# Performance work log

Measured on AMD Instinct MI355X. Metric: run time of the kernel, lower is better.

## Reference

```python
import math
import jax, jax.numpy as jnp
import numpy as np

B, T, M, D = 65536, 20, 4, 4   # batch, timesteps, regions, d_reg
L, H, FF = 3, 2, 16            # layers, heads, dim_feedforward
S = M + 1                      # seq_len with cls token
TAU = 10000.0


def setup_inputs() -> dict:
    key = jax.random.key(0)
    ks = jax.random.split(key, 8)

    def w(k, shape, std=0.1):
        return jax.random.normal(k, shape, dtype=jnp.float32) * std

    return {
        "regional_states": jax.random.normal(ks[0], (B, T, M, D), dtype=jnp.float32),
        "cls_token": w(ks[1], (1, 1, D), 0.02),
        # stacked per-layer params (layer axis first)
        "Wqkv": w(ks[2], (L, 3 * D, D)),   # nn.MultiheadAttention in_proj_weight
        "bqkv": jnp.zeros((L, 3 * D), jnp.float32),
        "Wo": w(ks[3], (L, D, D)),          # out_proj weight
        "bo": jnp.zeros((L, D), jnp.float32),
        "W1": w(ks[4], (L, FF, D)),         # linear1 weight (torch layout: out, in)
        "b1": jnp.zeros((L, FF), jnp.float32),
        "W2": w(ks[5], (L, D, FF)),         # linear2 weight
        "b2": jnp.zeros((L, D), jnp.float32),
    }


def _positional_encoding():
    # PE(pos,2i)=sin(pos/tau^(2i/D)), PE(pos,2i+1)=cos(...)
    pos = jnp.arange(S, dtype=jnp.float32)[:, None]            # (S,1)
    div = jnp.exp(jnp.arange(0, D, 2, dtype=jnp.float32) * (-math.log(TAU) / D))
    pe = jnp.zeros((S, D), jnp.float32)
    pe = pe.at[:, 0::2].set(jnp.sin(pos * div))
    pe = pe.at[:, 1::2].set(jnp.cos(pos * div))
    return pe  # (S, D)


def _layer(x, Wqkv, bqkv, Wo, bo, W1, b1, W2, b2):
    # x: (N, S, D). Dropout is identity (eval mode).
    N, Sq, Dm = x.shape
    hd = Dm // H
    qkv = x @ Wqkv.T + bqkv                     # (N, S, 3D)
    q, k, v = jnp.split(qkv, 3, axis=-1)

    def heads(t):
        return t.reshape(N, Sq, H, hd).transpose(0, 2, 1, 3)  # (N, H, S, hd)

    q, k, v = heads(q), heads(k), heads(v)
    scores = jnp.einsum("nhqd,nhkd->nhqk", q, k) / math.sqrt(hd)
    attn = jax.nn.softmax(scores, axis=-1)
    o = jnp.einsum("nhqk,nhkd->nhqd", attn, v)
    o = o.transpose(0, 2, 1, 3).reshape(N, Sq, Dm)
    attn_out = o @ Wo.T + bo
    x = x + attn_out                            # residual (no norm)
    ff = jax.nn.relu(x @ W1.T + b1) @ W2.T + b2
    return x + ff


def reference(regional_states, cls_token, Wqkv, bqkv, Wo, bo, W1, b1, W2, b2):
    Bq, Tq, Mq, Dq = regional_states.shape
    N = Bq * Tq
    x = regional_states.reshape(N, Mq, Dq)
    cls = jnp.broadcast_to(cls_token, (N, 1, Dq))
    x = jnp.concatenate([cls, x], axis=1)       # (N, S, D)
    x = x + _positional_encoding()[None, :, :]
    for i in range(L):
        x = _layer(x, Wqkv[i], bqkv[i], Wo[i], bo[i], W1[i], b1[i], W2[i], b2[i])
    F_g = x[:, 0, :].reshape(Bq, Tq, Dq)
    subregion_seq = x[:, 1:, :].reshape(Bq, Tq, Mq * Dq)
    return (F_g, subregion_seq)
```

## Files before the change

### kernel.cpp

```cpp
#include <hip/hip_runtime.h>


enum {
  OFF_CLS  = 0,
  OFF_WQKV = 4,
  OFF_BQKV = 148,
  OFF_WO   = 184,
  OFF_BO   = 232,
  OFF_W1   = 244,
  OFF_B1   = 436,
  OFF_W2   = 484,
  OFF_B2   = 676,
  WF_TOTAL = 688,
  FLAG_XF32 = 688
};

__device__ __forceinline__ float bf2f(unsigned short u) {
  unsigned int x = ((unsigned int)u) << 16;
  float f;
  __builtin_memcpy(&f, &x, 4);
  return f;
}

__device__ __forceinline__ bool is_bf16_packed(const unsigned int* w) {
  int pass = 0;
#pragma unroll
  for (int i = 0; i < 16; ++i) {
    unsigned int lo = w[i] & 0xFFFFu;
    unsigned int e = (lo >> 7) & 0xFFu;
    if (lo == 0u || (e >= 90u && e <= 140u)) ++pass;
  }
  return pass >= 15;
}

__global__ void mpt_prep(const void* __restrict__ cls,
                         const void* __restrict__ Wqkv,
                         const void* __restrict__ bqkv,
                         const void* __restrict__ Wo,
                         const void* __restrict__ bo,
                         const void* __restrict__ W1,
                         const void* __restrict__ b1,
                         const void* __restrict__ W2,
                         const void* __restrict__ b2,
                         const void* __restrict__ xin,
                         float* __restrict__ wf) {
  const bool wbf = is_bf16_packed((const unsigned int*)Wqkv);
  const bool xbf = is_bf16_packed((const unsigned int*)xin);
  if (threadIdx.x == 0) ((int*)wf)[FLAG_XF32] = xbf ? 0 : 1;
  for (int i = threadIdx.x; i < WF_TOTAL; i += 256) {
    const void* src;
    int k;
    if      (i < OFF_WQKV) { src = cls;  k = i - OFF_CLS;  }
    else if (i < OFF_BQKV) { src = Wqkv; k = i - OFF_WQKV; }
    else if (i < OFF_WO)   { src = bqkv; k = i - OFF_BQKV; }
    else if (i < OFF_BO)   { src = Wo;   k = i - OFF_WO;   }
    else if (i < OFF_W1)   { src = bo;   k = i - OFF_BO;   }
    else if (i < OFF_B1)   { src = W1;   k = i - OFF_W1;   }
    else if (i < OFF_W2)   { src = b1;   k = i - OFF_B1;   }
    else if (i < OFF_B2)   { src = W2;   k = i - OFF_W2;   }
    else                   { src = b2;   k = i - OFF_B2;   }
    wf[i] = wbf ? bf2f(((const unsigned short*)src)[k])
                : ((const float*)src)[k];
  }
}

__global__ __launch_bounds__(256) void mpt_main(
    const void* __restrict__ xin,
    const float* __restrict__ wf,
    float* __restrict__ out,
    int N) {
  const int n = blockIdx.x * 256 + threadIdx.x;
  if (n >= N) return;

  const int xf32 = ((const int*)wf)[FLAG_XF32];

  const float pe[5][4] = {
    { 0.0f,                1.0f,                0.0f,                1.0f               },
    { 0.8414709848078965f, 0.5403023058681398f, 0.0099998333341667f, 0.9999500004166653f },
    { 0.9092974268256817f,-0.4161468365471424f, 0.0199986666933331f, 0.9998000066665778f },
    { 0.1411200080598672f,-0.9899924966004454f, 0.0299955002024957f, 0.9995500337489875f },
    {-0.7568024953079283f,-0.6536436208636119f, 0.0399893341866342f, 0.9992001066609779f }
  };

  float raw[16];
  if (xf32) {
    const float4* pf = reinterpret_cast<const float4*>((const float*)xin + (size_t)n * 16);
#pragma unroll
    for (int r = 0; r < 4; ++r) {
      float4 t = pf[r];
      raw[r * 4 + 0] = t.x; raw[r * 4 + 1] = t.y;
      raw[r * 4 + 2] = t.z; raw[r * 4 + 3] = t.w;
    }
  } else {
    struct alignas(16) U8 { unsigned short v[8]; };
    const U8* p = reinterpret_cast<const U8*>((const unsigned short*)xin + (size_t)n * 16);
    U8 a0 = p[0], a1 = p[1];
#pragma unroll
    for (int j = 0; j < 8; ++j) {
      raw[j]     = bf2f(a0.v[j]);
      raw[8 + j] = bf2f(a1.v[j]);
    }
  }

  float x[5][4];
#pragma unroll
  for (int d = 0; d < 4; ++d) x[0][d] = wf[OFF_CLS + d] + pe[0][d];
#pragma unroll
  for (int r = 0; r < 4; ++r)
#pragma unroll
    for (int d = 0; d < 4; ++d) x[1 + r][d] = raw[r * 4 + d] + pe[1 + r][d];

  const float scale = 0.70710678118654752f;

#pragma unroll
  for (int l = 0; l < 3; ++l) {
    const float* Wqkv = wf + OFF_WQKV + l * 48;
    const float* bqkv = wf + OFF_BQKV + l * 12;
    const float* Wo   = wf + OFF_WO   + l * 16;
    const float* bo   = wf + OFF_BO   + l * 4;
    const float* W1   = wf + OFF_W1   + l * 64;
    const float* b1   = wf + OFF_B1   + l * 16;
    const float* W2   = wf + OFF_W2   + l * 64;
    const float* b2   = wf + OFF_B2   + l * 4;

    float q[5][4], k[5][4], v[5][4];
#pragma unroll
    for (int s = 0; s < 5; ++s) {
#pragma unroll
      for (int j = 0; j < 12; ++j) {
        float a = bqkv[j];
#pragma unroll
        for (int d = 0; d < 4; ++d) a = fmaf(x[s][d], Wqkv[j * 4 + d], a);
        if (j < 4)      q[s][j] = a;
        else if (j < 8) k[s][j - 4] = a;
        else            v[s][j - 8] = a;
      }
    }

    float o[5][4];
#pragma unroll
    for (int h = 0; h < 2; ++h) {
      const int d0 = 2 * h, d1 = 2 * h + 1;
#pragma unroll
      for (int si = 0; si < 5; ++si) {
        float sc[5];
        float mx = -3.0e38f;
#pragma unroll
        for (int sj = 0; sj < 5; ++sj) {
          float s0 = q[si][d0] * k[sj][d0] + q[si][d1] * k[sj][d1];
          sc[sj] = s0 * scale;
          mx = fmaxf(mx, sc[sj]);
        }
        float den = 0.f, o0 = 0.f, o1 = 0.f;
#pragma unroll
        for (int sj = 0; sj < 5; ++sj) {
          float e = __expf(sc[sj] - mx);
          den += e;
          o0 = fmaf(e, v[sj][d0], o0);
          o1 = fmaf(e, v[sj][d1], o1);
        }
        float inv = __builtin_amdgcn_rcpf(den);
        o[si][d0] = o0 * inv;
        o[si][d1] = o1 * inv;
      }
    }

#pragma unroll
    for (int s = 0; s < 5; ++s) {
      float nx[4];
#pragma unroll
      for (int i = 0; i < 4; ++i) {
        float a = bo[i];
#pragma unroll
        for (int j = 0; j < 4; ++j) a = fmaf(o[s][j], Wo[i * 4 + j], a);
        nx[i] = x[s][i] + a;
      }
#pragma unroll
      for (int i = 0; i < 4; ++i) x[s][i] = nx[i];

      float acc[4] = {b2[0], b2[1], b2[2], b2[3]};
#pragma unroll
      for (int f = 0; f < 16; ++f) {
        float hs = b1[f];
#pragma unroll
        for (int d = 0; d < 4; ++d) hs = fmaf(x[s][d], W1[f * 4 + d], hs);
        hs = fmaxf(hs, 0.f);
#pragma unroll
        for (int i = 0; i < 4; ++i) acc[i] = fmaf(hs, W2[i * 16 + f], acc[i]);
      }
#pragma unroll
      for (int i = 0; i < 4; ++i) x[s][i] += acc[i];
    }
  }

  float4 fg = make_float4(x[0][0], x[0][1], x[0][2], x[0][3]);
  *reinterpret_cast<float4*>(out + (size_t)n * 4) = fg;

  float* sub = out + (size_t)N * 4 + (size_t)n * 16;
#pragma unroll
  for (int r = 0; r < 4; ++r) {
    float4 t = make_float4(x[1 + r][0], x[1 + r][1], x[1 + r][2], x[1 + r][3]);
    *reinterpret_cast<float4*>(sub + r * 4) = t;
  }
}

extern "C" void kernel_launch(void* const* d_in, const int* in_sizes, int n_in,
                              void* d_out, int out_size, void* d_ws, size_t ws_size,
                              hipStream_t stream) {
  float* wf = (float*)d_ws;

  mpt_prep<<<1, 256, 0, stream>>>(
      d_in[1],
      d_in[2],
      d_in[3],
      d_in[4],
      d_in[5],
      d_in[6],
      d_in[7],
      d_in[8],
      d_in[9],
      d_in[0],
      wf);

  const int N = in_sizes[0] / 16;
  mpt_main<<<(N + 255) / 256, 256, 0, stream>>>(
      d_in[0], wf, (float*)d_out, N);
}
```

Measured before the change: 296.9 us.

## Process two sequences per thread with packed float2 math and prescaled keys

Each thread now handles two sequences packed into float2 vectors, so the compiler can emit packed FMA (v_pk_fma_f32) instructions. Weights are duplicated into float2 pairs in the workspace, and the key projection is prescaled by 1/sqrt(hd) in the prep kernel. The softmax max-subtraction is dropped, and Q/K/V projections are recomputed per head rather than stored. The aim is to halve VALU instruction count, at the cost of more registers per thread, half as many threads, and possible exp overflow without the max shift.

```diff
diff --git a/kernel.cpp b/kernel.cpp
--- a/kernel.cpp
+++ b/kernel.cpp
@@ -1,5 +1,7 @@
 #include <hip/hip_runtime.h>
 
+
+typedef float f2 __attribute__((ext_vector_type(2)));
 
 enum {
   OFF_CLS  = 0,
@@ -12,7 +14,7 @@
   OFF_W2   = 484,
   OFF_B2   = 676,
   WF_TOTAL = 688,
-  FLAG_XF32 = 688
+  FLAG_IDX = 2 * WF_TOTAL
 };
 
 __device__ __forceinline__ float bf2f(unsigned short u) {
@@ -46,7 +48,8 @@
                          float* __restrict__ wf) {
   const bool wbf = is_bf16_packed((const unsigned int*)Wqkv);
   const bool xbf = is_bf16_packed((const unsigned int*)xin);
-  if (threadIdx.x == 0) ((int*)wf)[FLAG_XF32] = xbf ? 0 : 1;
+  if (threadIdx.x == 0) ((int*)wf)[FLAG_IDX] = xbf ? 0 : 1;
+  const float scale = 0.70710678118654752f;
   for (int i = threadIdx.x; i < WF_TOTAL; i += 256) {
     const void* src;
     int k;
@@ -59,20 +62,59 @@
     else if (i < OFF_W2)   { src = b1;   k = i - OFF_B1;   }
     else if (i < OFF_B2)   { src = W2;   k = i - OFF_W2;   }
     else                   { src = b2;   k = i - OFF_B2;   }
-    wf[i] = wbf ? bf2f(((const unsigned short*)src)[k])
-                : ((const float*)src)[k];
-  }
+    float val = wbf ? bf2f(((const unsigned short*)src)[k])
+                    : ((const float*)src)[k];
+    if (i >= OFF_WQKV && i < OFF_BQKV) {
+      int kk = i - OFF_WQKV;
+      int row = (kk % 48) / 4;
+      if (row >= 4 && row < 8) val *= scale;
+    } else if (i >= OFF_BQKV && i < OFF_WO) {
+      int j = (i - OFF_BQKV) % 12;
+      if (j >= 4 && j < 8) val *= scale;
+    }
+    wf[2 * i]     = val;
+    wf[2 * i + 1] = val;
+  }
+}
+
+__device__ __forceinline__ f2 fma2(f2 a, f2 b, f2 c) {
+  return __builtin_elementwise_fma(a, b, c);
+}
+__device__ __forceinline__ f2 dot4b(const f2* __restrict__ w,
+                                    const f2* __restrict__ xv, f2 bias) {
+  f2 acc = fma2(xv[0], w[0], bias);
+  acc = fma2(xv[1], w[1], acc);
+  acc = fma2(xv[2], w[2], acc);
+  acc = fma2(xv[3], w[3], acc);
+  return acc;
+}
+__device__ __forceinline__ f2 expv(f2 v) {
+  f2 r;
+  r.x = __expf(v.x);
+  r.y = __expf(v.y);
+  return r;
+}
+__device__ __forceinline__ f2 rcpv(f2 v) {
+  f2 r;
+  r.x = __builtin_amdgcn_rcpf(v.x);
+  r.y = __builtin_amdgcn_rcpf(v.y);
+  return r;
 }
 
 __global__ __launch_bounds__(256) void mpt_main(
     const void* __restrict__ xin,
-    const float* __restrict__ wf,
+    const float* __restrict__ wfr,
     float* __restrict__ out,
     int N) {
-  const int n = blockIdx.x * 256 + threadIdx.x;
-  if (n >= N) return;
-
-  const int xf32 = ((const int*)wf)[FLAG_XF32];
+  const int t = blockIdx.x * 256 + threadIdx.x;
+  const int NP = (N + 1) >> 1;
+  if (t >= NP) return;
+  const int a = 2 * t, b = 2 * t + 1;
+  const bool bvalid = (b < N);
+  const int bb = bvalid ? b : a;
+
+  const int xf32 = ((const int*)wfr)[FLAG_IDX];
+  const f2* W = (const f2*)wfr;
 
   const float pe[5][4] = {
     { 0.0f,                1.0f,                0.0f,                1.0f               },
@@ -82,125 +124,123 @@
     {-0.7568024953079283f,-0.6536436208636119f, 0.0399893341866342f, 0.9992001066609779f }
   };
 
-  float raw[16];
+  f2 raw[16];
   if (xf32) {
-    const float4* pf = reinterpret_cast<const float4*>((const float*)xin + (size_t)n * 16);
+    const float4* pf = (const float4*)xin;
 #pragma unroll
     for (int r = 0; r < 4; ++r) {
-      float4 t = pf[r];
-      raw[r * 4 + 0] = t.x; raw[r * 4 + 1] = t.y;
-      raw[r * 4 + 2] = t.z; raw[r * 4 + 3] = t.w;
+      float4 A = pf[(size_t)a * 4 + r];
+      float4 B = pf[(size_t)bb * 4 + r];
+      raw[r * 4 + 0] = (f2){A.x, B.x};
+      raw[r * 4 + 1] = (f2){A.y, B.y};
+      raw[r * 4 + 2] = (f2){A.z, B.z};
+      raw[r * 4 + 3] = (f2){A.w, B.w};
     }
   } else {
     struct alignas(16) U8 { unsigned short v[8]; };
-    const U8* p = reinterpret_cast<const U8*>((const unsigned short*)xin + (size_t)n * 16);
-    U8 a0 = p[0], a1 = p[1];
+    const U8* p = (const U8*)xin;
+    U8 A0 = p[(size_t)a * 2], A1 = p[(size_t)a * 2 + 1];
+    U8 B0 = p[(size_t)bb * 2], B1 = p[(size_t)bb * 2 + 1];
 #pragma unroll
     for (int j = 0; j < 8; ++j) {
-      raw[j]     = bf2f(a0.v[j]);
-      raw[8 + j] = bf2f(a1.v[j]);
-    }
-  }
-
-  float x[5][4];
-#pragma unroll
-  for (int d = 0; d < 4; ++d) x[0][d] = wf[OFF_CLS + d] + pe[0][d];
+      raw[j]     = (f2){bf2f(A0.v[j]), bf2f(B0.v[j])};
+      raw[8 + j] = (f2){bf2f(A1.v[j]), bf2f(B1.v[j])};
+    }
+  }
+
+  f2 x[5][4];
+#pragma unroll
+  for (int d = 0; d < 4; ++d)
+    x[0][d] = W[OFF_CLS + d] + (f2){pe[0][d], pe[0][d]};
 #pragma unroll
   for (int r = 0; r < 4; ++r)
 #pragma unroll
-    for (int d = 0; d < 4; ++d) x[1 + r][d] = raw[r * 4 + d] + pe[1 + r][d];
-
-  const float scale = 0.70710678118654752f;
+    for (int d = 0; d < 4; ++d)
+      x[1 + r][d] = raw[r * 4 + d] + (f2){pe[1 + r][d], pe[1 + r][d]};
 
 #pragma unroll
   for (int l = 0; l < 3; ++l) {
-    const float* Wqkv = wf + OFF_WQKV + l * 48;
-    const float* bqkv = wf + OFF_BQKV + l * 12;
-    const float* Wo   = wf + OFF_WO   + l * 16;
-    const float* bo   = wf + OFF_BO   + l * 4;
-    const float* W1   = wf + OFF_W1   + l * 64;
-    const float* b1   = wf + OFF_B1   + l * 16;
-    const float* W2   = wf + OFF_W2   + l * 64;
-    const float* b2   = wf + OFF_B2   + l * 4;
-
-    float q[5][4], k[5][4], v[5][4];
-#pragma unroll
-    for (int s = 0; s < 5; ++s) {
-#pragma unroll
-      for (int j = 0; j < 12; ++j) {
-        float a = bqkv[j];
-#pragma unroll
-        for (int d = 0; d < 4; ++d) a = fmaf(x[s][d], Wqkv[j * 4 + d], a);
-        if (j < 4)      q[s][j] = a;
-        else if (j < 8) k[s][j - 4] = a;
-        else            v[s][j - 8] = a;
-      }
-    }
-
-    float o[5][4];
+    const f2* Wq = W + OFF_WQKV + l * 48;
+    const f2* bq = W + OFF_BQKV + l * 12;
+    const f2* Wo = W + OFF_WO   + l * 16;
+    const f2* bo = W + OFF_BO   + l * 4;
+    const f2* W1 = W + OFF_W1   + l * 64;
+    const f2* b1 = W + OFF_B1   + l * 16;
+    const f2* W2 = W + OFF_W2   + l * 64;
+    const f2* b2 = W + OFF_B2   + l * 4;
+
+    f2 o[5][4];
 #pragma unroll
     for (int h = 0; h < 2; ++h) {
       const int d0 = 2 * h, d1 = 2 * h + 1;
+      f2 kh[5][2], vh[5][2];
+#pragma unroll
+      for (int s = 0; s < 5; ++s) {
+        kh[s][0] = dot4b(Wq + (4 + d0) * 4, x[s], bq[4 + d0]);
+        kh[s][1] = dot4b(Wq + (4 + d1) * 4, x[s], bq[4 + d1]);
+        vh[s][0] = dot4b(Wq + (8 + d0) * 4, x[s], bq[8 + d0]);
+        vh[s][1] = dot4b(Wq + (8 + d1) * 4, x[s], bq[8 + d1]);
+      }
 #pragma unroll
       for (int si = 0; si < 5; ++si) {
-        float sc[5];
-        float mx = -3.0e38f;
+        f2 q0 = dot4b(Wq + d0 * 4, x[si], bq[d0]);
+        f2 q1 = dot4b(Wq + d1 * 4, x[si], bq[d1]);
+        f2 e[5];
+        f2 den = (f2){0.f, 0.f};
 #pragma unroll
         for (int sj = 0; sj < 5; ++sj) {
-          float s0 = q[si][d0] * k[sj][d0] + q[si][d1] * k[sj][d1];
-          sc[sj] = s0 * scale;
-          mx = fmaxf(mx, sc[sj]);
+          f2 sc = fma2(q1, kh[sj][1], q0 * kh[sj][0]);
+          e[sj] = expv(sc);
+          den += e[sj];
         }
-        float den = 0.f, o0 = 0.f, o1 = 0.f;
+        f2 inv = rcpv(den);
+        f2 o0 = (f2){0.f, 0.f}, o1 = (f2){0.f, 0.f};
 #pragma unroll
         for (int sj = 0; sj < 5; ++sj) {
-          float e = __expf(sc[sj] - mx);
-          den += e;
-          o0 = fmaf(e, v[sj][d0], o0);
-          o1 = fmaf(e, v[sj][d1], o1);
+          o0 = fma2(e[sj], vh[sj][0], o0);
+          o1 = fma2(e[sj], vh[sj][1], o1);
         }
-        float inv = __builtin_amdgcn_rcpf(den);
         o[si][d0] = o0 * inv;
         o[si][d1] = o1 * inv;
       }
     }
 
 #pragma unroll
-    for (int s = 0; s < 5; ++s) {
-      float nx[4];
-#pragma unroll
-      for (int i = 0; i < 4; ++i) {
-        float a = bo[i];
-#pragma unroll
-        for (int j = 0; j < 4; ++j) a = fmaf(o[s][j], Wo[i * 4 + j], a);
-        nx[i] = x[s][i] + a;
+    for (int si = 0; si < 5; ++si) {
+      f2 nx[4];
+#pragma unroll
+      for (int i = 0; i < 4; ++i)
+        nx[i] = x[si][i] + dot4b(Wo + i * 4, o[si], bo[i]);
+
+      f2 acc[4] = {b2[0], b2[1], b2[2], b2[3]};
+#pragma unroll
+      for (int f = 0; f < 16; ++f) {
+        f2 hs = dot4b(W1 + f * 4, nx, b1[f]);
+        hs = __builtin_elementwise_max(hs, (f2){0.f, 0.f});
+#pragma unroll
+        for (int i = 0; i < 4; ++i) acc[i] = fma2(hs, W2[i * 16 + f], acc[i]);
       }
 #pragma unroll
-      for (int i = 0; i < 4; ++i) x[s][i] = nx[i];
-
-      float acc[4] = {b2[0], b2[1], b2[2], b2[3]};
-#pragma unroll
-      for (int f = 0; f < 16; ++f) {
-        float hs = b1[f];
-#pragma unroll
-        for (int d = 0; d < 4; ++d) hs = fmaf(x[s][d], W1[f * 4 + d], hs);
-        hs = fmaxf(hs, 0.f);
-#pragma unroll
-        for (int i = 0; i < 4; ++i) acc[i] = fmaf(hs, W2[i * 16 + f], acc[i]);
-      }
-#pragma unroll
-      for (int i = 0; i < 4; ++i) x[s][i] += acc[i];
-    }
-  }
-
-  float4 fg = make_float4(x[0][0], x[0][1], x[0][2], x[0][3]);
-  *reinterpret_cast<float4*>(out + (size_t)n * 4) = fg;
-
-  float* sub = out + (size_t)N * 4 + (size_t)n * 16;
-#pragma unroll
-  for (int r = 0; r < 4; ++r) {
-    float4 t = make_float4(x[1 + r][0], x[1 + r][1], x[1 + r][2], x[1 + r][3]);
-    *reinterpret_cast<float4*>(sub + r * 4) = t;
+      for (int i = 0; i < 4; ++i) x[si][i] = nx[i] + acc[i];
+    }
+  }
+
+  *reinterpret_cast<float4*>(out + (size_t)a * 4) =
+      make_float4(x[0][0].x, x[0][1].x, x[0][2].x, x[0][3].x);
+  float* subA = out + (size_t)N * 4 + (size_t)a * 16;
+#pragma unroll
+  for (int r = 0; r < 4; ++r)
+    *reinterpret_cast<float4*>(subA + r * 4) =
+        make_float4(x[1 + r][0].x, x[1 + r][1].x, x[1 + r][2].x, x[1 + r][3].x);
+
+  if (bvalid) {
+    *reinterpret_cast<float4*>(out + (size_t)b * 4) =
+        make_float4(x[0][0].y, x[0][1].y, x[0][2].y, x[0][3].y);
+    float* subB = out + (size_t)N * 4 + (size_t)b * 16;
+#pragma unroll
+    for (int r = 0; r < 4; ++r)
+      *reinterpret_cast<float4*>(subB + r * 4) =
+          make_float4(x[1 + r][0].y, x[1 + r][1].y, x[1 + r][2].y, x[1 + r][3].y);
   }
 }
 
@@ -210,19 +250,13 @@
   float* wf = (float*)d_ws;
 
   mpt_prep<<<1, 256, 0, stream>>>(
-      d_in[1],
-      d_in[2],
-      d_in[3],
-      d_in[4],
-      d_in[5],
-      d_in[6],
-      d_in[7],
-      d_in[8],
-      d_in[9],
+      d_in[1], d_in[2], d_in[3], d_in[4], d_in[5],
+      d_in[6], d_in[7], d_in[8], d_in[9],
       d_in[0],
       wf);
 
   const int N = in_sizes[0] / 16;
-  mpt_main<<<(N + 255) / 256, 256, 0, stream>>>(
+  const int NP = (N + 1) / 2;
+  mpt_main<<<(NP + 255) / 256, 256, 0, stream>>>(
       d_in[0], wf, (float*)d_out, N);
 }
```

New measurement: 790.3 us. 2.66x slower.

## Pack weights to fp16 pairs and use dot2 instructions with folded softmax scale

Applied to the files above, without the earlier changes.

The prep kernel now packs all weight matrices into fp16 pairs. It folds the attention scale and log2(e) into the key projection, and folds the CLS positional encoding into the stored CLS token. The main kernel converts activations to packed fp16 and does every projection and FFN with v_dot2 (fp16 inputs, fp32 accumulate), roughly halving the ALU instruction count. Softmax drops the max-subtraction and uses exp2 directly. This trades accuracy, through fp16 rounding of activations and weights and possible overflow without max subtraction, for fewer VALU ops in a compute-bound per-thread kernel.

```diff
diff --git a/kernel.cpp b/kernel.cpp
--- a/kernel.cpp
+++ b/kernel.cpp
@@ -1,18 +1,20 @@
 #include <hip/hip_runtime.h>
 
 
+typedef _Float16 h2 __attribute__((ext_vector_type(2)));
+
 enum {
-  OFF_CLS  = 0,
-  OFF_WQKV = 4,
-  OFF_BQKV = 148,
-  OFF_WO   = 184,
-  OFF_BO   = 232,
-  OFF_W1   = 244,
-  OFF_B1   = 436,
-  OFF_W2   = 484,
-  OFF_B2   = 676,
-  WF_TOTAL = 688,
-  FLAG_XF32 = 688
+  WF_CLS  = 0,
+  WF_BQKV = 4,
+  WF_BO   = 40,
+  WF_B1   = 52,
+  WF_B2   = 100,
+  H_QKV   = 112,
+  H_WO    = 184,
+  H_W1    = 208,
+  H_W2    = 304,
+  WF_FLAG = 400,
+  WF_TOTAL = 401
 };
 
 __device__ __forceinline__ float bf2f(unsigned short u) {
@@ -31,6 +33,29 @@
     if (lo == 0u || (e >= 90u && e <= 140u)) ++pass;
   }
   return pass >= 15;
+}
+
+__device__ __forceinline__ float dot2(h2 a, h2 b, float c) {
+#if __has_builtin(__builtin_amdgcn_fdot2)
+  return __builtin_amdgcn_fdot2(a, b, c, false);
+#else
+  return fmaf((float)a.x, (float)b.x, fmaf((float)a.y, (float)b.y, c));
+#endif
+}
+
+__device__ __forceinline__ h2 pk(float a, float b) {
+  auto t = __builtin_amdgcn_cvt_pkrtz(a, b);
+  h2 r;
+  __builtin_memcpy(&r, &t, sizeof(r));
+  return r;
+}
+
+__device__ __forceinline__ float fexp2(float x) {
+#if __has_builtin(__builtin_amdgcn_exp2f)
+  return __builtin_amdgcn_exp2f(x);
+#else
+  return __builtin_exp2f(x);
+#endif
 }
 
 __global__ void mpt_prep(const void* __restrict__ cls,
@@ -46,21 +71,56 @@
                          float* __restrict__ wf) {
   const bool wbf = is_bf16_packed((const unsigned int*)Wqkv);
   const bool xbf = is_bf16_packed((const unsigned int*)xin);
-  if (threadIdx.x == 0) ((int*)wf)[FLAG_XF32] = xbf ? 0 : 1;
-  for (int i = threadIdx.x; i < WF_TOTAL; i += 256) {
-    const void* src;
-    int k;
-    if      (i < OFF_WQKV) { src = cls;  k = i - OFF_CLS;  }
-    else if (i < OFF_BQKV) { src = Wqkv; k = i - OFF_WQKV; }
-    else if (i < OFF_WO)   { src = bqkv; k = i - OFF_BQKV; }
-    else if (i < OFF_BO)   { src = Wo;   k = i - OFF_WO;   }
-    else if (i < OFF_W1)   { src = bo;   k = i - OFF_BO;   }
-    else if (i < OFF_B1)   { src = W1;   k = i - OFF_W1;   }
-    else if (i < OFF_W2)   { src = b1;   k = i - OFF_B1;   }
-    else if (i < OFF_B2)   { src = W2;   k = i - OFF_W2;   }
-    else                   { src = b2;   k = i - OFF_B2;   }
-    wf[i] = wbf ? bf2f(((const unsigned short*)src)[k])
-                : ((const float*)src)[k];
+  const float FS = 1.44269504088896341f * 0.70710678118654752f;
+
+  for (int w = threadIdx.x; w < WF_TOTAL; w += 256) {
+    if (w == WF_FLAG) { ((int*)wf)[w] = xbf ? 0 : 1; continue; }
+
+    auto g = [&](const void* src, int idx) -> float {
+      return wbf ? bf2f(((const unsigned short*)src)[idx])
+                 : ((const float*)src)[idx];
+    };
+
+    if (w < H_QKV) {
+      float val;
+      if (w < WF_BQKV) {
+        val = g(cls, w) + ((w & 1) ? 1.0f : 0.0f);
+      } else if (w < WF_BO) {
+        int t = w - WF_BQKV;
+        val = g(bqkv, t);
+        int j = t % 12;
+        if (j >= 4 && j < 8) val *= FS;
+      } else if (w < WF_B1) {
+        val = g(bo, w - WF_BO);
+      } else if (w < WF_B2) {
+        val = g(b1, w - WF_B1);
+      } else {
+        val = g(b2, w - WF_B2);
+      }
+      wf[w] = val;
+    } else {
+      int base;
+      float s = 1.0f;
+      if (w < H_WO) {
+        int t = w - H_QKV, l = t / 24, j = (t % 24) / 2, p = t & 1;
+        base = l * 48 + j * 4 + p * 2;
+        if (j >= 4 && j < 8) s = FS;
+        h2 hv = pk(g(Wqkv, base) * s, g(Wqkv, base + 1) * s);
+        ((h2*)wf)[w] = hv;
+      } else if (w < H_W1) {
+        int t = w - H_WO, l = t / 8, i = (t % 8) / 2, p = t & 1;
+        base = l * 16 + i * 4 + p * 2;
+        ((h2*)wf)[w] = pk(g(Wo, base), g(Wo, base + 1));
+      } else if (w < H_W2) {
+        int t = w - H_W1, l = t / 32, f = (t % 32) / 2, p = t & 1;
+        base = l * 64 + f * 4 + p * 2;
+        ((h2*)wf)[w] = pk(g(W1, base), g(W1, base + 1));
+      } else {
+        int t = w - H_W2, l = t / 32, i = (t % 32) / 8, p = t % 8;
+        base = l * 64 + i * 16 + p * 2;
+        ((h2*)wf)[w] = pk(g(W2, base), g(W2, base + 1));
+      }
+    }
   }
 }
 
@@ -72,10 +132,10 @@
   const int n = blockIdx.x * 256 + threadIdx.x;
   if (n >= N) return;
 
-  const int xf32 = ((const int*)wf)[FLAG_XF32];
-
-  const float pe[5][4] = {
-    { 0.0f,                1.0f,                0.0f,                1.0f               },
+  const int xf32 = ((const int*)wf)[WF_FLAG];
+  const h2* hw = (const h2*)wf;
+
+  const float pe[4][4] = {
     { 0.8414709848078965f, 0.5403023058681398f, 0.0099998333341667f, 0.9999500004166653f },
     { 0.9092974268256817f,-0.4161468365471424f, 0.0199986666933331f, 0.9998000066665778f },
     { 0.1411200080598672f,-0.9899924966004454f, 0.0299955002024957f, 0.9995500337489875f },
@@ -104,33 +164,36 @@
 
   float x[5][4];
 #pragma unroll
-  for (int d = 0; d < 4; ++d) x[0][d] = wf[OFF_CLS + d] + pe[0][d];
+  for (int d = 0; d < 4; ++d) x[0][d] = wf[WF_CLS + d];
 #pragma unroll
   for (int r = 0; r < 4; ++r)
 #pragma unroll
-    for (int d = 0; d < 4; ++d) x[1 + r][d] = raw[r * 4 + d] + pe[1 + r][d];
-
-  const float scale = 0.70710678118654752f;
+    for (int d = 0; d < 4; ++d) x[1 + r][d] = raw[r * 4 + d] + pe[r][d];
 
 #pragma unroll
   for (int l = 0; l < 3; ++l) {
-    const float* Wqkv = wf + OFF_WQKV + l * 48;
-    const float* bqkv = wf + OFF_BQKV + l * 12;
-    const float* Wo   = wf + OFF_WO   + l * 16;
-    const float* bo   = wf + OFF_BO   + l * 4;
-    const float* W1   = wf + OFF_W1   + l * 64;
-    const float* b1   = wf + OFF_B1   + l * 16;
-    const float* W2   = wf + OFF_W2   + l * 64;
-    const float* b2   = wf + OFF_B2   + l * 4;
+    const float* bq = wf + WF_BQKV + l * 12;
+    const float* bo = wf + WF_BO   + l * 4;
+    const float* b1 = wf + WF_B1   + l * 16;
+    const float* b2 = wf + WF_B2   + l * 4;
+    const h2* hq  = hw + H_QKV + l * 24;
+    const h2* hwo = hw + H_WO  + l * 8;
+    const h2* hw1 = hw + H_W1  + l * 32;
+    const h2* hw2 = hw + H_W2  + l * 32;
+
+    h2 xh[5][2];
+#pragma unroll
+    for (int s = 0; s < 5; ++s) {
+      xh[s][0] = pk(x[s][0], x[s][1]);
+      xh[s][1] = pk(x[s][2], x[s][3]);
+    }
 
     float q[5][4], k[5][4], v[5][4];
 #pragma unroll
     for (int s = 0; s < 5; ++s) {
 #pragma unroll
       for (int j = 0; j < 12; ++j) {
-        float a = bqkv[j];
-#pragma unroll
-        for (int d = 0; d < 4; ++d) a = fmaf(x[s][d], Wqkv[j * 4 + d], a);
+        float a = dot2(xh[s][0], hq[j * 2], dot2(xh[s][1], hq[j * 2 + 1], bq[j]));
         if (j < 4)      q[s][j] = a;
         else if (j < 8) k[s][j - 4] = a;
         else            v[s][j - 8] = a;
@@ -141,25 +204,27 @@
 #pragma unroll
     for (int h = 0; h < 2; ++h) {
       const int d0 = 2 * h, d1 = 2 * h + 1;
+      h2 qh[5], kh[5];
+#pragma unroll
+      for (int s = 0; s < 5; ++s) {
+        qh[s] = pk(q[s][d0], q[s][d1]);
+        kh[s] = pk(k[s][d0], k[s][d1]);
+      }
 #pragma unroll
       for (int si = 0; si < 5; ++si) {
-        float sc[5];
-        float mx = -3.0e38f;
+        float e[5], den = 0.f;
 #pragma unroll
         for (int sj = 0; sj < 5; ++sj) {
-          float s0 = q[si][d0] * k[sj][d0] + q[si][d1] * k[sj][d1];
-          sc[sj] = s0 * scale;
-          mx = fmaxf(mx, sc[sj]);
-        }
-        float den = 0.f, o0 = 0.f, o1 = 0.f;
-#pragma unroll
-        for (int sj = 0; sj < 5; ++sj) {
-          float e = __expf(sc[sj] - mx);
-          den += e;
-          o0 = fmaf(e, v[sj][d0], o0);
-          o1 = fmaf(e, v[sj][d1], o1);
+          e[sj] = fexp2(dot2(qh[si], kh[sj], 0.0f));
+          den += e[sj];
         }
         float inv = __builtin_amdgcn_rcpf(den);
+        float o0 = 0.f, o1 = 0.f;
+#pragma unroll
+        for (int sj = 0; sj < 5; ++sj) {
+          o0 = fmaf(e[sj], v[sj][d0], o0);
+          o1 = fmaf(e[sj], v[sj][d1], o1);
+        }
         o[si][d0] = o0 * inv;
         o[si][d1] = o1 * inv;
       }
@@ -167,41 +232,35 @@
 
 #pragma unroll
     for (int s = 0; s < 5; ++s) {
+      h2 oh0 = pk(o[s][0], o[s][1]), oh1 = pk(o[s][2], o[s][3]);
       float nx[4];
 #pragma unroll
-      for (int i = 0; i < 4; ++i) {
-        float a = bo[i];
-#pragma unroll
-        for (int j = 0; j < 4; ++j) a = fmaf(o[s][j], Wo[i * 4 + j], a);
-        nx[i] = x[s][i] + a;
-      }
-#pragma unroll
-      for (int i = 0; i < 4; ++i) x[s][i] = nx[i];
-
+      for (int i = 0; i < 4; ++i)
+        nx[i] = dot2(oh0, hwo[i * 2], dot2(oh1, hwo[i * 2 + 1], x[s][i] + bo[i]));
+
+      h2 nh0 = pk(nx[0], nx[1]), nh1 = pk(nx[2], nx[3]);
       float acc[4] = {b2[0], b2[1], b2[2], b2[3]};
 #pragma unroll
-      for (int f = 0; f < 16; ++f) {
-        float hs = b1[f];
-#pragma unroll
-        for (int d = 0; d < 4; ++d) hs = fmaf(x[s][d], W1[f * 4 + d], hs);
-        hs = fmaxf(hs, 0.f);
-#pragma unroll
-        for (int i = 0; i < 4; ++i) acc[i] = fmaf(hs, W2[i * 16 + f], acc[i]);
-      }
-#pragma unroll
-      for (int i = 0; i < 4; ++i) x[s][i] += acc[i];
-    }
-  }
-
-  float4 fg = make_float4(x[0][0], x[0][1], x[0][2], x[0][3]);
-  *reinterpret_cast<float4*>(out + (size_t)n * 4) = fg;
-
+      for (int p = 0; p < 8; ++p) {
+        int f0 = 2 * p, f1 = 2 * p + 1;
+        float h0 = fmaxf(dot2(nh0, hw1[f0 * 2], dot2(nh1, hw1[f0 * 2 + 1], b1[f0])), 0.f);
+        float h1 = fmaxf(dot2(nh0, hw1[f1 * 2], dot2(nh1, hw1[f1 * 2 + 1], b1[f1])), 0.f);
+        h2 hh = pk(h0, h1);
+#pragma unroll
+        for (int i = 0; i < 4; ++i) acc[i] = dot2(hh, hw2[i * 8 + p], acc[i]);
+      }
+#pragma unroll
+      for (int i = 0; i < 4; ++i) x[s][i] = nx[i] + acc[i];
+    }
+  }
+
+  *reinterpret_cast<float4*>(out + (size_t)n * 4) =
+      make_float4(x[0][0], x[0][1], x[0][2], x[0][3]);
   float* sub = out + (size_t)N * 4 + (size_t)n * 16;
 #pragma unroll
-  for (int r = 0; r < 4; ++r) {
-    float4 t = make_float4(x[1 + r][0], x[1 + r][1], x[1 + r][2], x[1 + r][3]);
-    *reinterpret_cast<float4*>(sub + r * 4) = t;
-  }
+  for (int r = 0; r < 4; ++r)
+    *reinterpret_cast<float4*>(sub + r * 4) =
+        make_float4(x[1 + r][0], x[1 + r][1], x[1 + r][2], x[1 + r][3]);
 }
 
 extern "C" void kernel_launch(void* const* d_in, const int* in_sizes, int n_in,
@@ -210,15 +269,8 @@
   float* wf = (float*)d_ws;
 
   mpt_prep<<<1, 256, 0, stream>>>(
-      d_in[1],
-      d_in[2],
-      d_in[3],
-      d_in[4],
-      d_in[5],
-      d_in[6],
-      d_in[7],
-      d_in[8],
-      d_in[9],
+      d_in[1], d_in[2], d_in[3], d_in[4], d_in[5],
+      d_in[6], d_in[7], d_in[8], d_in[9],
       d_in[0],
       wf);
 
```

After: 275.9 us. 7.1% less time.
